# Kernel optimization log

Measured on AMD Instinct MI355X. Metric: run time of the kernel, lower is better.

Reference implementation:

```python
import jax, jax.numpy as jnp
import numpy as np

EMBED_DIM = 1024
NUM_HEADS = 16
HEAD_DIM = EMBED_DIM // NUM_HEADS
B, QL, CL = 2, 2048, 2048


def setup_inputs() -> dict:
    key = jax.random.key(0)
    ks = jax.random.split(key, 10)
    s = 1.0 / np.sqrt(EMBED_DIM)  # torch Linear default init scale (approx)
    inp = {
        "query": jax.random.normal(ks[0], (B, QL, EMBED_DIM), jnp.float32),
        "context": jax.random.normal(ks[1], (B, CL, EMBED_DIM), jnp.float32),
        "Wq": jax.random.normal(ks[2], (EMBED_DIM, EMBED_DIM), jnp.float32) * s,
        "bq": jnp.zeros((EMBED_DIM,), jnp.float32),
        "Wk": jax.random.normal(ks[3], (EMBED_DIM, EMBED_DIM), jnp.float32) * s,
        "bk": jnp.zeros((EMBED_DIM,), jnp.float32),
        "Wv": jax.random.normal(ks[4], (EMBED_DIM, EMBED_DIM), jnp.float32) * s,
        "bv": jnp.zeros((EMBED_DIM,), jnp.float32),
        "Wo": jax.random.normal(ks[5], (EMBED_DIM, EMBED_DIM), jnp.float32) * s,
        "bo": jnp.zeros((EMBED_DIM,), jnp.float32),
    }
    return inp


def reference(query, context, Wq, bq, Wk, bk, Wv, bv, Wo, bo):
    b, ql, _ = query.shape
    cl = context.shape[1]
    # projections (torch Linear: x @ W.T + b; here W stored as (in, out) so x @ W + b)
    Q = (query @ Wq + bq).reshape(b, ql, NUM_HEADS, HEAD_DIM).transpose(0, 2, 1, 3)
    K = (context @ Wk + bk).reshape(b, cl, NUM_HEADS, HEAD_DIM).transpose(0, 2, 1, 3)
    V = (context @ Wv + bv).reshape(b, cl, NUM_HEADS, HEAD_DIM).transpose(0, 2, 1, 3)
    # scores [b, h, ql, cl]
    scores = jnp.einsum("bhqd,bhkd->bhqk", Q, K) / np.sqrt(HEAD_DIM).astype(np.float32)
    probs = jax.nn.softmax(scores, axis=-1)
    # dropout=0.0 (eval): identity
    attended = jnp.einsum("bhqk,bhkd->bhqd", probs, V)
    attended = attended.transpose(0, 2, 1, 3).reshape(b, ql, EMBED_DIM)
    return attended @ Wo + bo
```

## Files before the change

### kernel.cpp

```cpp
#include <hip/hip_runtime.h>
#include <hip/hip_bf16.h>
#include <stdint.h>

#define EMBED 1024
#define NH 16
#define HD 64
#define BATCH 2
#define QLEN 2048
#define CLEN 2048

typedef short short8 __attribute__((ext_vector_type(8)));
typedef unsigned short ushort8v __attribute__((ext_vector_type(8)));
typedef float f32x4 __attribute__((ext_vector_type(4)));
typedef float f32x16 __attribute__((ext_vector_type(16)));
typedef uint32_t u32x4 __attribute__((ext_vector_type(4)));

__device__ __forceinline__ void async_load16(const void* g, void* l) {
    __builtin_amdgcn_global_load_lds((const __attribute__((address_space(1))) void*)g,
                                     (__attribute__((address_space(3))) void*)l, 16, 0, 0);
}

__device__ __forceinline__ uint32_t pack2(float a, float b) {
    float2 f{a, b};
    __hip_bfloat162 t = __float22bfloat162_rn(f);
    uint32_t u;
    __builtin_memcpy(&u, &t, 4);
    return u;
}

__global__ void cvt_two(const float* __restrict__ a, __hip_bfloat16* __restrict__ oa,
                        const float* __restrict__ b2, __hip_bfloat16* __restrict__ ob) {
    const float* src = blockIdx.y ? b2 : a;
    __hip_bfloat16* dst = blockIdx.y ? ob : oa;
    int i = (blockIdx.x * 256 + threadIdx.x) * 4;
    float4 v = *(const float4*)(src + i);
    __hip_bfloat16 h[4];
    h[0] = __float2bfloat16(v.x);
    h[1] = __float2bfloat16(v.y);
    h[2] = __float2bfloat16(v.z);
    h[3] = __float2bfloat16(v.w);
    *(ushort4*)(dst + i) = *(const ushort4*)h;
}

__global__ void wtrans4(const float* __restrict__ W0, const float* __restrict__ W1,
                        const float* __restrict__ W2, const float* __restrict__ W3,
                        __hip_bfloat16* __restrict__ T0, __hip_bfloat16* __restrict__ T1,
                        __hip_bfloat16* __restrict__ T2, __hip_bfloat16* __restrict__ T3) {
    const int z = blockIdx.z;
    const float* W = z == 0 ? W0 : z == 1 ? W1 : z == 2 ? W2 : W3;
    __hip_bfloat16* Wt = z == 0 ? T0 : z == 1 ? T1 : z == 2 ? T2 : T3;
    __shared__ float t[32][33];
    const int tx = threadIdx.x, ty = threadIdx.y;
    const int n0 = blockIdx.x * 32, k0 = blockIdx.y * 32;
#pragma unroll
    for (int r = 0; r < 4; r++)
        t[ty * 4 + r][tx] = W[(size_t)(k0 + ty * 4 + r) * EMBED + n0 + tx];
    __syncthreads();
#pragma unroll
    for (int r = 0; r < 4; r++)
        Wt[(size_t)(n0 + ty * 4 + r) * EMBED + k0 + tx] = __float2bfloat16(t[tx][ty * 4 + r]);
}

__global__ __launch_bounds__(256) void vtrans(const __hip_bfloat16* __restrict__ V,
                                              __hip_bfloat16* __restrict__ Vt) {
    __shared__ unsigned short t[64][65];
    const int tid = threadIdx.x;
    const int c0 = blockIdx.x * 64;
    const int b = blockIdx.y >> 4, h = blockIdx.y & 15;
    const int r = tid >> 2;
    const int cs = (tid & 3) * 16;
    const unsigned short* src = (const unsigned short*)V + (size_t)(b * CLEN + c0 + r) * EMBED + h * HD + cs;
    ushort8v v0 = *(const ushort8v*)src;
    ushort8v v1 = *(const ushort8v*)(src + 8);
#pragma unroll
    for (int j = 0; j < 8; j++) { t[r][cs + j] = v0[j]; t[r][cs + 8 + j] = v1[j]; }
    __syncthreads();
    const int d = tid >> 2;
    const int ts = (tid & 3) * 16;
    ushort8v o0, o1;
#pragma unroll
    for (int j = 0; j < 8; j++) { o0[j] = t[ts + j][d]; o1[j] = t[ts + 8 + j][d]; }
    unsigned short* dst = (unsigned short*)Vt + (size_t)((b * NH + h) * HD + d) * CLEN + c0 + ts;
    *(ushort8v*)dst = o0;
    *(ushort8v*)(dst + 8) = o1;
}

__device__ __forceinline__ void store_val(float v, __hip_bfloat16* p) { *p = __float2bfloat16(v); }
__device__ __forceinline__ void store_val(float v, float* p) { *p = v; }

template <typename OutT>
__device__ __forceinline__ void gemm128_body(
    const __hip_bfloat16* __restrict__ A, const __hip_bfloat16* __restrict__ Bt,
    const float* __restrict__ bias, OutT* __restrict__ C,
    int N, int m0, int n0, int cb,
    __hip_bfloat16* As, __hip_bfloat16* Bs) {
    const int K = EMBED;
    const int tid = threadIdx.x;
    const int wave = __builtin_amdgcn_readfirstlane(tid >> 6);
    const int lane = tid & 63, l15 = lane & 15, quad = lane >> 4;
    const int wm = (wave >> 1) * 64, wn = (wave & 1) * 64;
    const int srow = tid >> 2, sseg = (tid & 3) * 8;
    f32x4 acc[4][4] = {};
    for (int k0 = 0; k0 < K; k0 += 32) {
        __syncthreads();
#pragma unroll
        for (int s = 0; s < 2; s++) {
            async_load16(A + (size_t)(m0 + s * 64 + srow) * K + k0 + sseg,
                         As + (size_t)(s * 256 + wave * 64) * 8);
            async_load16(Bt + (size_t)(n0 + s * 64 + srow) * K + k0 + sseg,
                         Bs + (size_t)(s * 256 + wave * 64) * 8);
        }
        __syncthreads();
        short8 af[4], bf[4];
#pragma unroll
        for (int t = 0; t < 4; t++) {
            af[t] = *(const short8*)(As + (wm + t * 16 + l15) * 32 + quad * 8);
            bf[t] = *(const short8*)(Bs + (wn + t * 16 + l15) * 32 + quad * 8);
        }
#pragma unroll
        for (int mt = 0; mt < 4; mt++)
#pragma unroll
            for (int nt = 0; nt < 4; nt++)
                acc[mt][nt] = __builtin_amdgcn_mfma_f32_16x16x32_bf16(af[mt], bf[nt], acc[mt][nt], 0, 0, 0);
    }
#pragma unroll
    for (int mt = 0; mt < 4; mt++) {
#pragma unroll
        for (int nt = 0; nt < 4; nt++) {
            const int c = cb + wn + nt * 16 + l15;
            const float bvv = bias[c];
            const int r0 = m0 + wm + mt * 16 + quad * 4;
#pragma unroll
            for (int r = 0; r < 4; r++)
                store_val(acc[mt][nt][r] + bvv, C + (size_t)(r0 + r) * N + c);
        }
    }
}

__global__ __launch_bounds__(256, 3) void proj128(
    const __hip_bfloat16* __restrict__ qbf, const __hip_bfloat16* __restrict__ cbf,
    const __hip_bfloat16* __restrict__ Wqt, const __hip_bfloat16* __restrict__ Wkvt,
    const float* __restrict__ bq, const float* __restrict__ bk, const float* __restrict__ bv,
    __hip_bfloat16* __restrict__ Qp, __hip_bfloat16* __restrict__ Kp, __hip_bfloat16* __restrict__ Vp) {
    __shared__ __hip_bfloat16 As[128 * 32];
    __shared__ __hip_bfloat16 Bs[128 * 32];
    const int blk = blockIdx.x;
    const __hip_bfloat16 *A, *Bt;
    int m0, n0;
    if (blk < 256) {
        A = qbf; Bt = Wqt; m0 = (blk >> 3) * 128; n0 = (blk & 7) * 128;
    } else {
        const int f = blk - 256;
        A = cbf; Bt = Wkvt; m0 = (f >> 4) * 128; n0 = (f & 15) * 128;
    }
    const float* bias;
    __hip_bfloat16* C;
    int cb;
    if (blk < 256) { bias = bq; C = Qp; cb = n0; }
    else if (n0 < 1024) { bias = bk; C = Kp; cb = n0; }
    else { bias = bv; C = Vp; cb = n0 - 1024; }
    gemm128_body<__hip_bfloat16>(A, Bt, bias, C, 1024, m0, n0, cb, As, Bs);
}

__global__ __launch_bounds__(256, 4) void oproj(
    const __hip_bfloat16* __restrict__ A, const __hip_bfloat16* __restrict__ Bt,
    const float* __restrict__ bias, float* __restrict__ C) {
    __shared__ __hip_bfloat16 As[64 * 32];
    __shared__ __hip_bfloat16 Bs[128 * 32];
    const int K = EMBED, N = EMBED;
    const int m0 = blockIdx.y * 64, n0 = blockIdx.x * 128;
    const int tid = threadIdx.x;
    const int wave = __builtin_amdgcn_readfirstlane(tid >> 6);
    const int lane = tid & 63, l15 = lane & 15, quad = lane >> 4;
    const int wm = (wave & 1) * 32, wn = (wave >> 1) * 64;
    const int srow = tid >> 2, sseg = (tid & 3) * 8;
    f32x4 acc[2][4] = {};
    for (int k0 = 0; k0 < K; k0 += 32) {
        __syncthreads();
        async_load16(A + (size_t)(m0 + srow) * K + k0 + sseg, As + (size_t)(wave * 64) * 8);
#pragma unroll
        for (int s = 0; s < 2; s++)
            async_load16(Bt + (size_t)(n0 + s * 64 + srow) * K + k0 + sseg,
                         Bs + (size_t)(s * 256 + wave * 64) * 8);
        __syncthreads();
        short8 af[2], bf[4];
#pragma unroll
        for (int t = 0; t < 2; t++)
            af[t] = *(const short8*)(As + (wm + t * 16 + l15) * 32 + quad * 8);
#pragma unroll
        for (int t = 0; t < 4; t++)
            bf[t] = *(const short8*)(Bs + (wn + t * 16 + l15) * 32 + quad * 8);
#pragma unroll
        for (int mt = 0; mt < 2; mt++)
#pragma unroll
            for (int nt = 0; nt < 4; nt++)
                acc[mt][nt] = __builtin_amdgcn_mfma_f32_16x16x32_bf16(af[mt], bf[nt], acc[mt][nt], 0, 0, 0);
    }
#pragma unroll
    for (int mt = 0; mt < 2; mt++) {
#pragma unroll
        for (int nt = 0; nt < 4; nt++) {
            const int c = n0 + wn + nt * 16 + l15;
            const float bvv = bias[c];
            const int r0 = m0 + wm + mt * 16 + quad * 4;
#pragma unroll
            for (int r = 0; r < 4; r++)
                C[(size_t)(r0 + r) * N + c] = acc[mt][nt][r] + bvv;
        }
    }
}

__global__ __launch_bounds__(128, 2) void flash_attn(
    const __hip_bfloat16* __restrict__ Q, const __hip_bfloat16* __restrict__ K,
    const __hip_bfloat16* __restrict__ Vt, __hip_bfloat16* __restrict__ O) {
    __shared__ __hip_bfloat16 Ks[64 * 64];
    __shared__ __hip_bfloat16 Vs[64 * 64];
    const int tid = threadIdx.x;
    const int wq = __builtin_amdgcn_readfirstlane(tid >> 6);
    const int lane = tid & 63;
    const int l31 = lane & 31;
    const int hbit = lane >> 5;
    const int b = blockIdx.y >> 4, h = blockIdx.y & 15;
    const int q0 = blockIdx.x * 64;
    const size_t kbase = (size_t)b * CLEN * EMBED + (size_t)h * HD;
    const size_t vtbase = (size_t)((b * NH + h) * HD) * CLEN;
    const int srow = tid >> 3;
    const int sg = (tid & 7) ^ (srow & 7);
    const int ldsoff = (tid & 64) * 8;

    const __hip_bfloat16* qptr =
        Q + (size_t)(b * QLEN + q0 + wq * 32 + l31) * EMBED + h * HD + hbit * 8;
    short8 qf[4];
#pragma unroll
    for (int t = 0; t < 4; t++) qf[t] = *(const short8*)(qptr + t * 16);

    f32x16 o[2] = {};
    float lsum = 0.f;
    const float CEXP = 0.125f * 1.44269504f;

    for (int c0 = 0; c0 < CLEN; c0 += 64) {
        __syncthreads();
#pragma unroll
        for (int i = 0; i < 4; i++) {
            async_load16(K + kbase + (size_t)(c0 + i * 16 + srow) * EMBED + sg * 8,
                         Ks + i * 1024 + ldsoff);
            async_load16(Vt + vtbase + (size_t)(i * 16 + srow) * CLEN + c0 + sg * 8,
                         Vs + i * 1024 + ldsoff);
        }
        __syncthreads();

#pragma unroll
        for (int mc = 0; mc < 2; mc++) {
            const int row = mc * 32 + l31;
            const __hip_bfloat16* kr = Ks + row * 64;
            f32x16 s = {};
#pragma unroll
            for (int kc = 0; kc < 4; kc++) {
                short8 kf = *(const short8*)(kr + ((2 * kc + hbit) ^ (row & 7)) * 8);
                s = __builtin_amdgcn_mfma_f32_32x32x16_bf16(kf, qf[kc], s, 0, 0, 0);
            }
            uint32_t dw[8];
#pragma unroll
            for (int i = 0; i < 8; i++) {
                const float p0 = __builtin_amdgcn_exp2f(s[2 * i] * CEXP);
                const float p1 = __builtin_amdgcn_exp2f(s[2 * i + 1] * CEXP);
                lsum += p0 + p1;
                dw[i] = pack2(p0, p1);
            }
#pragma unroll
            for (int tp = 0; tp < 2; tp++) {
                const uint32_t a0 = hbit ? dw[4 * tp + 2] : dw[4 * tp + 0];
                const uint32_t a1 = hbit ? dw[4 * tp + 3] : dw[4 * tp + 1];
                const uint32_t b0 = hbit ? dw[4 * tp + 0] : dw[4 * tp + 2];
                const uint32_t b1 = hbit ? dw[4 * tp + 1] : dw[4 * tp + 3];
                const uint32_t x0 = (uint32_t)__shfl_xor((int)b0, 32);
                const uint32_t x1 = (uint32_t)__shfl_xor((int)b1, 32);
                u32x4 fb;
                fb[0] = hbit ? x0 : a0;
                fb[1] = hbit ? x1 : a1;
                fb[2] = hbit ? a0 : x0;
                fb[3] = hbit ? a1 : x1;
                const short8 pfr = __builtin_bit_cast(short8, fb);
                const int kc = mc * 2 + tp;
#pragma unroll
                for (int dm = 0; dm < 2; dm++) {
                    const int vrow = dm * 32 + l31;
                    short8 vf = *(const short8*)(Vs + vrow * 64 + ((2 * kc + hbit) ^ (vrow & 7)) * 8);
                    o[dm] = __builtin_amdgcn_mfma_f32_32x32x16_bf16(vf, pfr, o[dm], 0, 0, 0);
                }
            }
        }
    }

    lsum += __shfl_xor(lsum, 32);
    const float inv = 1.0f / lsum;
    const int q = q0 + wq * 32 + l31;
    __hip_bfloat16* orow = O + (size_t)(b * QLEN + q) * EMBED + h * HD;
#pragma unroll
    for (int dm = 0; dm < 2; dm++) {
#pragma unroll
        for (int g = 0; g < 4; g++) {
            __hip_bfloat16 ob[4];
#pragma unroll
            for (int r = 0; r < 4; r++) ob[r] = __float2bfloat16(o[dm][g * 4 + r] * inv);
            *(ushort4*)(orow + dm * 32 + hbit * 4 + g * 8) = *(const ushort4*)ob;
        }
    }
}

extern "C" void kernel_launch(void* const* d_in, const int* in_sizes, int n_in,
                              void* d_out, int out_size, void* d_ws, size_t ws_size,
                              hipStream_t stream) {
    const float* query = (const float*)d_in[0];
    const float* context = (const float*)d_in[1];
    const float* Wq = (const float*)d_in[2];
    const float* bq = (const float*)d_in[3];
    const float* Wk = (const float*)d_in[4];
    const float* bk = (const float*)d_in[5];
    const float* Wv = (const float*)d_in[6];
    const float* bv = (const float*)d_in[7];
    const float* Wo = (const float*)d_in[8];
    const float* bo = (const float*)d_in[9];
    float* out = (float*)d_out;

    const int NTOK = BATCH * QLEN;
    const int NACT = NTOK * EMBED;
    const int NW = EMBED * EMBED;

    __hip_bfloat16* qbf = (__hip_bfloat16*)d_ws;
    __hip_bfloat16* cbf = qbf + NACT;
    __hip_bfloat16* Wqt = cbf + NACT;
    __hip_bfloat16* Wkt = Wqt + NW;
    __hip_bfloat16* Wvt = Wkt + NW;
    __hip_bfloat16* Wot = Wvt + NW;
    __hip_bfloat16* Qp = Wot + NW;
    __hip_bfloat16* Kp = Qp + NACT;
    __hip_bfloat16* Vtr = Kp + NACT;
    __hip_bfloat16* att = Vtr + NACT;

    cvt_two<<<dim3(NACT / 1024, 2), 256, 0, stream>>>(query, qbf, context, cbf);
    wtrans4<<<dim3(32, 32, 4), dim3(32, 8), 0, stream>>>(Wq, Wk, Wv, Wo, Wqt, Wkt, Wvt, Wot);

    proj128<<<768, 256, 0, stream>>>(qbf, cbf, Wqt, Wkt, bq, bk, bv, Qp, Kp, att);

    vtrans<<<dim3(CLEN / 64, BATCH * NH), 256, 0, stream>>>(att, Vtr);

    flash_attn<<<dim3(QLEN / 64, BATCH * NH), 128, 0, stream>>>(Qp, Kp, Vtr, att);

    oproj<<<dim3(EMBED / 128, NTOK / 64), 256, 0, stream>>>(att, Wot, bo, out);
}
```

Before: 227.8 us.

## Fuse prep kernels, write V transposed from projection, split-KV flash attention

Merges the activation conversion and weight transposes into one prep launch, and has the projection kernel write V directly in transposed layout, which removes the separate vtrans kernel. Flash attention now uses 256 threads, with two wave pairs each covering half of the context. Their partial outputs and row sums are combined through shared memory at the end. This cuts launches and a full round trip of V through memory, and doubles the waves working on each query tile. The cost is strided 8-byte V stores and a shared-memory reduction step.

```diff
diff --git a/kernel.cpp b/kernel.cpp
--- a/kernel.cpp
+++ b/kernel.cpp
@@ -10,7 +10,6 @@
 #define CLEN 2048
 
 typedef short short8 __attribute__((ext_vector_type(8)));
-typedef unsigned short ushort8v __attribute__((ext_vector_type(8)));
 typedef float f32x4 __attribute__((ext_vector_type(4)));
 typedef float f32x16 __attribute__((ext_vector_type(16)));
 typedef uint32_t u32x4 __attribute__((ext_vector_type(4)));
@@ -28,79 +27,54 @@
     return u;
 }
 
-__global__ void cvt_two(const float* __restrict__ a, __hip_bfloat16* __restrict__ oa,
-                        const float* __restrict__ b2, __hip_bfloat16* __restrict__ ob) {
-    const float* src = blockIdx.y ? b2 : a;
-    __hip_bfloat16* dst = blockIdx.y ? ob : oa;
-    int i = (blockIdx.x * 256 + threadIdx.x) * 4;
-    float4 v = *(const float4*)(src + i);
-    __hip_bfloat16 h[4];
-    h[0] = __float2bfloat16(v.x);
-    h[1] = __float2bfloat16(v.y);
-    h[2] = __float2bfloat16(v.z);
-    h[3] = __float2bfloat16(v.w);
-    *(ushort4*)(dst + i) = *(const ushort4*)h;
-}
-
-__global__ void wtrans4(const float* __restrict__ W0, const float* __restrict__ W1,
-                        const float* __restrict__ W2, const float* __restrict__ W3,
-                        __hip_bfloat16* __restrict__ T0, __hip_bfloat16* __restrict__ T1,
-                        __hip_bfloat16* __restrict__ T2, __hip_bfloat16* __restrict__ T3) {
-    const int z = blockIdx.z;
-    const float* W = z == 0 ? W0 : z == 1 ? W1 : z == 2 ? W2 : W3;
-    __hip_bfloat16* Wt = z == 0 ? T0 : z == 1 ? T1 : z == 2 ? T2 : T3;
-    __shared__ float t[32][33];
-    const int tx = threadIdx.x, ty = threadIdx.y;
-    const int n0 = blockIdx.x * 32, k0 = blockIdx.y * 32;
-#pragma unroll
-    for (int r = 0; r < 4; r++)
-        t[ty * 4 + r][tx] = W[(size_t)(k0 + ty * 4 + r) * EMBED + n0 + tx];
-    __syncthreads();
-#pragma unroll
-    for (int r = 0; r < 4; r++)
-        Wt[(size_t)(n0 + ty * 4 + r) * EMBED + k0 + tx] = __float2bfloat16(t[tx][ty * 4 + r]);
-}
-
-__global__ __launch_bounds__(256) void vtrans(const __hip_bfloat16* __restrict__ V,
-                                              __hip_bfloat16* __restrict__ Vt) {
-    __shared__ unsigned short t[64][65];
-    const int tid = threadIdx.x;
-    const int c0 = blockIdx.x * 64;
-    const int b = blockIdx.y >> 4, h = blockIdx.y & 15;
-    const int r = tid >> 2;
-    const int cs = (tid & 3) * 16;
-    const unsigned short* src = (const unsigned short*)V + (size_t)(b * CLEN + c0 + r) * EMBED + h * HD + cs;
-    ushort8v v0 = *(const ushort8v*)src;
-    ushort8v v1 = *(const ushort8v*)(src + 8);
-#pragma unroll
-    for (int j = 0; j < 8; j++) { t[r][cs + j] = v0[j]; t[r][cs + 8 + j] = v1[j]; }
-    __syncthreads();
-    const int d = tid >> 2;
-    const int ts = (tid & 3) * 16;
-    ushort8v o0, o1;
-#pragma unroll
-    for (int j = 0; j < 8; j++) { o0[j] = t[ts + j][d]; o1[j] = t[ts + 8 + j][d]; }
-    unsigned short* dst = (unsigned short*)Vt + (size_t)((b * NH + h) * HD + d) * CLEN + c0 + ts;
-    *(ushort8v*)dst = o0;
-    *(ushort8v*)(dst + 8) = o1;
-}
-
-__device__ __forceinline__ void store_val(float v, __hip_bfloat16* p) { *p = __float2bfloat16(v); }
-__device__ __forceinline__ void store_val(float v, float* p) { *p = v; }
-
-template <typename OutT>
-__device__ __forceinline__ void gemm128_body(
+__global__ void prep(const float* __restrict__ query, const float* __restrict__ context,
+                     __hip_bfloat16* __restrict__ qbf, __hip_bfloat16* __restrict__ cbf,
+                     const float* __restrict__ W0, const float* __restrict__ W1,
+                     const float* __restrict__ W2, const float* __restrict__ W3,
+                     __hip_bfloat16* __restrict__ T0, __hip_bfloat16* __restrict__ T1,
+                     __hip_bfloat16* __restrict__ T2, __hip_bfloat16* __restrict__ T3) {
+    const int y = blockIdx.y;
+    const int tid = threadIdx.x;
+    if (y < 2) {
+        const float* src = y ? context : query;
+        __hip_bfloat16* dst = y ? cbf : qbf;
+#pragma unroll
+        for (int k = 0; k < 4; k++) {
+            const int i = (blockIdx.x * 1024 + k * 256 + tid) * 4;
+            float4 v = *(const float4*)(src + i);
+            __hip_bfloat16 h[4];
+            h[0] = __float2bfloat16(v.x);
+            h[1] = __float2bfloat16(v.y);
+            h[2] = __float2bfloat16(v.z);
+            h[3] = __float2bfloat16(v.w);
+            *(ushort4*)(dst + i) = *(const ushort4*)h;
+        }
+    } else {
+        const int z = y - 2;
+        const float* W = z == 0 ? W0 : z == 1 ? W1 : z == 2 ? W2 : W3;
+        __hip_bfloat16* Wt = z == 0 ? T0 : z == 1 ? T1 : z == 2 ? T2 : T3;
+        __shared__ float t[32][33];
+        const int tx = tid & 31, ty = tid >> 5;
+        const int n0 = (blockIdx.x & 31) * 32, k0 = (blockIdx.x >> 5) * 32;
+#pragma unroll
+        for (int r = 0; r < 4; r++)
+            t[ty * 4 + r][tx] = W[(size_t)(k0 + ty * 4 + r) * EMBED + n0 + tx];
+        __syncthreads();
+#pragma unroll
+        for (int r = 0; r < 4; r++)
+            Wt[(size_t)(n0 + ty * 4 + r) * EMBED + k0 + tx] = __float2bfloat16(t[tx][ty * 4 + r]);
+    }
+}
+
+__device__ __forceinline__ void gemm128_acc(
     const __hip_bfloat16* __restrict__ A, const __hip_bfloat16* __restrict__ Bt,
-    const float* __restrict__ bias, OutT* __restrict__ C,
-    int N, int m0, int n0, int cb,
-    __hip_bfloat16* As, __hip_bfloat16* Bs) {
+    int m0, int n0, __hip_bfloat16* As, __hip_bfloat16* Bs, f32x4 acc[4][4]) {
     const int K = EMBED;
     const int tid = threadIdx.x;
     const int wave = __builtin_amdgcn_readfirstlane(tid >> 6);
     const int lane = tid & 63, l15 = lane & 15, quad = lane >> 4;
     const int wm = (wave >> 1) * 64, wn = (wave & 1) * 64;
     const int srow = tid >> 2, sseg = (tid & 3) * 8;
-    f32x4 acc[4][4] = {};
     for (int k0 = 0; k0 < K; k0 += 32) {
         __syncthreads();
 #pragma unroll
@@ -123,25 +97,13 @@
             for (int nt = 0; nt < 4; nt++)
                 acc[mt][nt] = __builtin_amdgcn_mfma_f32_16x16x32_bf16(af[mt], bf[nt], acc[mt][nt], 0, 0, 0);
     }
-#pragma unroll
-    for (int mt = 0; mt < 4; mt++) {
-#pragma unroll
-        for (int nt = 0; nt < 4; nt++) {
-            const int c = cb + wn + nt * 16 + l15;
-            const float bvv = bias[c];
-            const int r0 = m0 + wm + mt * 16 + quad * 4;
-#pragma unroll
-            for (int r = 0; r < 4; r++)
-                store_val(acc[mt][nt][r] + bvv, C + (size_t)(r0 + r) * N + c);
-        }
-    }
 }
 
 __global__ __launch_bounds__(256, 3) void proj128(
     const __hip_bfloat16* __restrict__ qbf, const __hip_bfloat16* __restrict__ cbf,
     const __hip_bfloat16* __restrict__ Wqt, const __hip_bfloat16* __restrict__ Wkvt,
     const float* __restrict__ bq, const float* __restrict__ bk, const float* __restrict__ bv,
-    __hip_bfloat16* __restrict__ Qp, __hip_bfloat16* __restrict__ Kp, __hip_bfloat16* __restrict__ Vp) {
+    __hip_bfloat16* __restrict__ Qp, __hip_bfloat16* __restrict__ Kp, __hip_bfloat16* __restrict__ Vtr) {
     __shared__ __hip_bfloat16 As[128 * 32];
     __shared__ __hip_bfloat16 Bs[128 * 32];
     const int blk = blockIdx.x;
@@ -153,13 +115,47 @@
         const int f = blk - 256;
         A = cbf; Bt = Wkvt; m0 = (f >> 4) * 128; n0 = (f & 15) * 128;
     }
-    const float* bias;
-    __hip_bfloat16* C;
-    int cb;
-    if (blk < 256) { bias = bq; C = Qp; cb = n0; }
-    else if (n0 < 1024) { bias = bk; C = Kp; cb = n0; }
-    else { bias = bv; C = Vp; cb = n0 - 1024; }
-    gemm128_body<__hip_bfloat16>(A, Bt, bias, C, 1024, m0, n0, cb, As, Bs);
+    f32x4 acc[4][4] = {};
+    gemm128_acc(A, Bt, m0, n0, As, Bs, acc);
+
+    const int tid = threadIdx.x;
+    const int wave = __builtin_amdgcn_readfirstlane(tid >> 6);
+    const int lane = tid & 63, l15 = lane & 15, quad = lane >> 4;
+    const int wm = (wave >> 1) * 64, wn = (wave & 1) * 64;
+
+    if (blk >= 256 && n0 >= 1024) {
+        const int cb = n0 - 1024;
+        const int b2 = m0 >> 11;
+        const int tokbase = (m0 & 2047) + wm;
+#pragma unroll
+        for (int mt = 0; mt < 4; mt++) {
+#pragma unroll
+            for (int nt = 0; nt < 4; nt++) {
+                const int col = cb + wn + nt * 16 + l15;
+                const float bvv = bv[col];
+                const int tok = tokbase + mt * 16 + quad * 4;
+                __hip_bfloat16 vb[4];
+#pragma unroll
+                for (int r = 0; r < 4; r++) vb[r] = __float2bfloat16(acc[mt][nt][r] + bvv);
+                *(ushort4*)(Vtr + (size_t)(b2 * 1024 + col) * CLEN + tok) = *(const ushort4*)vb;
+            }
+        }
+    } else {
+        const float* bias = (blk < 256) ? bq : bk;
+        __hip_bfloat16* C = (blk < 256) ? Qp : Kp;
+#pragma unroll
+        for (int mt = 0; mt < 4; mt++) {
+#pragma unroll
+            for (int nt = 0; nt < 4; nt++) {
+                const int c = n0 + wn + nt * 16 + l15;
+                const float bvv = bias[c];
+                const int r0 = m0 + wm + mt * 16 + quad * 4;
+#pragma unroll
+                for (int r = 0; r < 4; r++)
+                    C[(size_t)(r0 + r) * 1024 + c] = __float2bfloat16(acc[mt][nt][r] + bvv);
+            }
+        }
+    }
 }
 
 __global__ __launch_bounds__(256, 4) void oproj(
@@ -210,23 +206,23 @@
     }
 }
 
-__global__ __launch_bounds__(128, 2) void flash_attn(
+__global__ __launch_bounds__(256, 4) void flash_attn(
     const __hip_bfloat16* __restrict__ Q, const __hip_bfloat16* __restrict__ K,
     const __hip_bfloat16* __restrict__ Vt, __hip_bfloat16* __restrict__ O) {
-    __shared__ __hip_bfloat16 Ks[64 * 64];
-    __shared__ __hip_bfloat16 Vs[64 * 64];
-    const int tid = threadIdx.x;
-    const int wq = __builtin_amdgcn_readfirstlane(tid >> 6);
-    const int lane = tid & 63;
-    const int l31 = lane & 31;
-    const int hbit = lane >> 5;
+    __shared__ __hip_bfloat16 Ks[2][64 * 64];
+    __shared__ __hip_bfloat16 Vs[2][64 * 64];
+    const int tid = threadIdx.x;
+    const int wave = __builtin_amdgcn_readfirstlane(tid >> 6);
+    const int wq = wave & 1, wc = wave >> 1;
+    const int lane = tid & 63, l31 = lane & 31, hbit = lane >> 5;
     const int b = blockIdx.y >> 4, h = blockIdx.y & 15;
     const int q0 = blockIdx.x * 64;
     const size_t kbase = (size_t)b * CLEN * EMBED + (size_t)h * HD;
     const size_t vtbase = (size_t)((b * NH + h) * HD) * CLEN;
-    const int srow = tid >> 3;
-    const int sg = (tid & 7) ^ (srow & 7);
-    const int ldsoff = (tid & 64) * 8;
+    const int srow8 = lane >> 3;
+    const int sg = (lane & 7) ^ srow8;
+    __hip_bfloat16* stK = Ks[wc];
+    __hip_bfloat16* stV = Vs[wc];
 
     const __hip_bfloat16* qptr =
         Q + (size_t)(b * QLEN + q0 + wq * 32 + l31) * EMBED + h * HD + hbit * 8;
@@ -237,22 +233,28 @@
     f32x16 o[2] = {};
     float lsum = 0.f;
     const float CEXP = 0.125f * 1.44269504f;
-
-    for (int c0 = 0; c0 < CLEN; c0 += 64) {
-        __syncthreads();
-#pragma unroll
-        for (int i = 0; i < 4; i++) {
-            async_load16(K + kbase + (size_t)(c0 + i * 16 + srow) * EMBED + sg * 8,
-                         Ks + i * 1024 + ldsoff);
-            async_load16(Vt + vtbase + (size_t)(i * 16 + srow) * CLEN + c0 + sg * 8,
-                         Vs + i * 1024 + ldsoff);
+    const int cbase = wc * (CLEN / 2);
+
+    for (int t = 0; t < 16; ++t) {
+        const int c0 = cbase + t * 64;
+        __syncthreads();
+        if (wq == 0) {
+#pragma unroll
+            for (int i = 0; i < 8; i++)
+                async_load16(K + kbase + (size_t)(c0 + i * 8 + srow8) * EMBED + sg * 8,
+                             stK + i * 512);
+        } else {
+#pragma unroll
+            for (int i = 0; i < 8; i++)
+                async_load16(Vt + vtbase + (size_t)(i * 8 + srow8) * CLEN + c0 + sg * 8,
+                             stV + i * 512);
         }
         __syncthreads();
 
 #pragma unroll
         for (int mc = 0; mc < 2; mc++) {
             const int row = mc * 32 + l31;
-            const __hip_bfloat16* kr = Ks + row * 64;
+            const __hip_bfloat16* kr = stK + row * 64;
             f32x16 s = {};
 #pragma unroll
             for (int kc = 0; kc < 4; kc++) {
@@ -281,29 +283,56 @@
                 fb[2] = hbit ? a0 : x0;
                 fb[3] = hbit ? a1 : x1;
                 const short8 pfr = __builtin_bit_cast(short8, fb);
-                const int kc = mc * 2 + tp;
+                const int kc2 = mc * 2 + tp;
 #pragma unroll
                 for (int dm = 0; dm < 2; dm++) {
                     const int vrow = dm * 32 + l31;
-                    short8 vf = *(const short8*)(Vs + vrow * 64 + ((2 * kc + hbit) ^ (vrow & 7)) * 8);
+                    short8 vf = *(const short8*)(stV + vrow * 64 + ((2 * kc2 + hbit) ^ (vrow & 7)) * 8);
                     o[dm] = __builtin_amdgcn_mfma_f32_32x32x16_bf16(vf, pfr, o[dm], 0, 0, 0);
                 }
             }
         }
     }
 
-    lsum += __shfl_xor(lsum, 32);
-    const float inv = 1.0f / lsum;
-    const int q = q0 + wq * 32 + l31;
-    __hip_bfloat16* orow = O + (size_t)(b * QLEN + q) * EMBED + h * HD;
-#pragma unroll
-    for (int dm = 0; dm < 2; dm++) {
-#pragma unroll
-        for (int g = 0; g < 4; g++) {
-            __hip_bfloat16 ob[4];
-#pragma unroll
-            for (int r = 0; r < 4; r++) ob[r] = __float2bfloat16(o[dm][g * 4 + r] * inv);
-            *(ushort4*)(orow + dm * 32 + hbit * 4 + g * 8) = *(const ushort4*)ob;
+    __syncthreads();
+    float4* scr4 = (float4*)&Ks[0][0];
+    float* scrl = (float*)&Vs[0][0];
+    if (wc == 1) {
+#pragma unroll
+        for (int i = 0; i < 8; i++) {
+            float4 c4;
+            c4.x = o[i >> 2][(i & 3) * 4 + 0];
+            c4.y = o[i >> 2][(i & 3) * 4 + 1];
+            c4.z = o[i >> 2][(i & 3) * 4 + 2];
+            c4.w = o[i >> 2][(i & 3) * 4 + 3];
+            scr4[i * 128 + wq * 64 + lane] = c4;
+        }
+        scrl[wq * 64 + lane] = lsum;
+    }
+    __syncthreads();
+    if (wc == 0) {
+        lsum += scrl[wq * 64 + lane];
+#pragma unroll
+        for (int i = 0; i < 8; i++) {
+            float4 p = scr4[i * 128 + wq * 64 + lane];
+            o[i >> 2][(i & 3) * 4 + 0] += p.x;
+            o[i >> 2][(i & 3) * 4 + 1] += p.y;
+            o[i >> 2][(i & 3) * 4 + 2] += p.z;
+            o[i >> 2][(i & 3) * 4 + 3] += p.w;
+        }
+        lsum += __shfl_xor(lsum, 32);
+        const float inv = 1.0f / lsum;
+        const int q = q0 + wq * 32 + l31;
+        __hip_bfloat16* orow = O + (size_t)(b * QLEN + q) * EMBED + h * HD;
+#pragma unroll
+        for (int dm = 0; dm < 2; dm++) {
+#pragma unroll
+            for (int g = 0; g < 4; g++) {
+                __hip_bfloat16 ob[4];
+#pragma unroll
+                for (int r = 0; r < 4; r++) ob[r] = __float2bfloat16(o[dm][g * 4 + r] * inv);
+                *(ushort4*)(orow + dm * 32 + hbit * 4 + g * 8) = *(const ushort4*)ob;
+            }
         }
     }
 }
@@ -338,14 +367,12 @@
     __hip_bfloat16* Vtr = Kp + NACT;
     __hip_bfloat16* att = Vtr + NACT;
 
-    cvt_two<<<dim3(NACT / 1024, 2), 256, 0, stream>>>(query, qbf, context, cbf);
-    wtrans4<<<dim3(32, 32, 4), dim3(32, 8), 0, stream>>>(Wq, Wk, Wv, Wo, Wqt, Wkt, Wvt, Wot);
-
-    proj128<<<768, 256, 0, stream>>>(qbf, cbf, Wqt, Wkt, bq, bk, bv, Qp, Kp, att);
-
-    vtrans<<<dim3(CLEN / 64, BATCH * NH), 256, 0, stream>>>(att, Vtr);
-
-    flash_attn<<<dim3(QLEN / 64, BATCH * NH), 128, 0, stream>>>(Qp, Kp, Vtr, att);
+    prep<<<dim3(1024, 6), 256, 0, stream>>>(query, context, qbf, cbf,
+                                            Wq, Wk, Wv, Wo, Wqt, Wkt, Wvt, Wot);
+
+    proj128<<<768, 256, 0, stream>>>(qbf, cbf, Wqt, Wkt, bq, bk, bv, Qp, Kp, Vtr);
+
+    flash_attn<<<dim3(QLEN / 64, BATCH * NH), 256, 0, stream>>>(Qp, Kp, Vtr, att);
 
     oproj<<<dim3(EMBED / 128, NTOK / 64), 256, 0, stream>>>(att, Wot, bo, out);
 }
```

After: 212.3 us. 6.8% less time.
